# Optimization experiments

Measured on AMD Instinct MI355X. Metric: run time of the kernel, lower is better.

The kernel has to match this reference:

```python
import jax, jax.numpy as jnp
import numpy as np
from jax import lax

B, CIN, H, W = 8, 64, 128, 128
COUT, K, STRIDE, PAD = 128, 3, 1, 1
NLEV = 256  # 2**activation_bits == 2**weight_bits


def setup_inputs() -> dict:
    key = jax.random.key(0)
    kx, kw = jax.random.split(key)
    x = jax.random.uniform(kx, (B, CIN, H, W), dtype=jnp.float32)
    weight = jax.random.normal(kw, (COUT, CIN, K, K), dtype=jnp.float32)
    bias = jnp.zeros((COUT,), dtype=jnp.float32)
    return {"x": x, "weight": weight, "bias": bias}


def _lut_table(weight):
    # quantized weights in [0, 255], integer-valued
    qw = jnp.clip(jnp.round(weight * (NLEV - 1)), 0, NLEV - 1).astype(jnp.int32)
    iv = jnp.arange(NLEV, dtype=jnp.int32)
    # emulate torch .to(int16) wraparound (qw*i can exceed 32767)
    lut = (qw[..., None] * iv).astype(jnp.int16)          # [O, C, K, K, 256]
    # the original sums pcilt over its (c,p,q) dims for EVERY patch entry;
    # precollapse those dims: T[i, o] = sum_{c,p,q} lut[o,c,p,q,i]
    T = lut.astype(jnp.int32).sum(axis=(1, 2, 3))          # [O, 256]
    return T.T                                             # [256, O]


def reference(x, weight, bias):
    T = _lut_table(weight)                                 # [256, COUT]
    xq = jnp.clip(jnp.round(x * (NLEV - 1)), 0, NLEV - 1).astype(jnp.int32)
    xp = jnp.pad(xq, ((0, 0), (0, 0), (PAD, PAD), (PAD, PAD)))  # zero-pad; T[:,0]=0 matches
    xc = jnp.moveaxis(xp, 1, 0)                            # [CIN, B, Hp, Wp]

    # accumulate per-pixel channel sum of LUT rows: A[b,h,w,o] = sum_c T[x[b,c,h,w], o]
    A0 = jnp.zeros((xp.shape[0], xp.shape[2], xp.shape[3], COUT), dtype=jnp.int32)

    def body(acc, ch):
        return acc + T[ch], None

    A, _ = lax.scan(body, A0, xc)                          # [B, Hp, Wp, COUT]

    # k x k sliding-window sum over spatial dims = sum over all patch entries
    out = lax.reduce_window(A.astype(jnp.float32), 0.0, lax.add,
                            (1, K, K, 1), (1, STRIDE, STRIDE, 1), 'VALID')
    out = jnp.moveaxis(out, 3, 1) + bias[None, :, None, None]  # [B, COUT, OH, OW]
    return out
```

## Files before the change

kernel.cpp:

```cpp
#include <hip/hip_runtime.h>

#define CIN   64
#define HW    128
#define COUT  128
#define TH    8
#define TW    32
#define PXR   34
#define NITER (TH + 2)
#define NTHR  512
#define HSTR  144
#define AKSTR 136
#define SLOT  (PXR * HSTR)

#define HM_OFF    0
#define KT_OFF    19584
#define SX_OFF    35968
#define SXP_OFF   36608
#define LDS_BYTES 39872

typedef int v4i __attribute__((ext_vector_type(4)));

__device__ __forceinline__ void wg_barrier() {
  asm volatile("s_waitcnt lgkmcnt(0)\n\ts_barrier" ::: "memory");
}

__device__ __forceinline__ int quad_sum(int v) {
  v += __builtin_amdgcn_mov_dpp(v, 0xB1, 0xF, 0xF, true);
  v += __builtin_amdgcn_mov_dpp(v, 0x4E, 0xF, 0xF, true);
  return v;
}

__global__ __launch_bounds__(512)
void build_tables(const float* __restrict__ weight, int* __restrict__ W_tab,
                  char* __restrict__ Kt_g) {
  __shared__ int qw_s[576];
  __shared__ int red_s[144];
  const int o = blockIdx.x;
  const int t = threadIdx.x;
  for (int j = t; j < 576; j += 512) {
    float w = weight[o * 576 + j];
    int q = (int)rintf(w * 255.f);
    qw_s[j] = q < 0 ? 0 : (q > 255 ? 255 : q);
  }
  __syncthreads();
  const int v = t >> 2, part = t & 3;
  const int i = 128 + v;
  int cnt = 0;
  const int j0 = part * 144;
  for (int j = j0; j < j0 + 144; ++j) cnt += (qw_s[j] * i) > 32767 ? 1 : 0;
  cnt = quad_sum(cnt);
  if (part == 0) Kt_g[o * 128 + v] = (char)(cnt - 128);
  if (t < 144)
    red_s[t] = qw_s[t * 4] + qw_s[t * 4 + 1] + qw_s[t * 4 + 2] + qw_s[t * 4 + 3];
  __syncthreads();
  if (t == 0) {
    int s = 0;
    for (int kk = 0; kk < 144; ++kk) s += red_s[kk];
    W_tab[o] = s;
  }
}

__global__ __launch_bounds__(NTHR, 4)
void pcilt_main(const float* __restrict__ x, const float* __restrict__ bias,
                const int* __restrict__ W_tab, const char* __restrict__ Kt_g,
                float* __restrict__ out) {
  __shared__ uint4 ldsv[LDS_BYTES / 16];
  char* ldsb = (char*)ldsv;
  unsigned char* HmB  = (unsigned char*)(ldsb + HM_OFF);
  unsigned char* KtB  = (unsigned char*)(ldsb + KT_OFF);
  unsigned short* AK  = (unsigned short*)(ldsb + KT_OFF);
  int* Sx             = (int*)(ldsb + SX_OFF);
  int* Sxp            = (int*)(ldsb + SXP_OFF);

  const int t   = (int)threadIdx.x;
  const int bid = (int)blockIdx.x;
  const int b  = bid & 7;
  const int k  = bid >> 3;
  const int h0 = (k >> 2) * TH;
  const int w0 = (k & 3) * TW;

  for (int i = t; i < 4096; i += NTHR)
    ((unsigned int*)KtB)[i] = ((const unsigned int*)Kt_g)[i];
  {
    const uint4 z4 = make_uint4(0, 0, 0, 0);
    for (int i = t; i < 4 * SLOT / 16; i += NTHR) ((uint4*)HmB)[i] = z4;
  }

  const int l    = t & 15;
  const int slot = t >> 4;
  const int w    = t >> 6;
  const int kq   = (t >> 4) & 3;
  const int we   = t & 31;
  const int og   = t >> 5;

  float wf[8], bi[8];
#pragma unroll
  for (int m = 0; m < 8; ++m) {
    wf[m] = (float)W_tab[og * 8 + m];
    bi[m] = bias[og * 8 + m];
  }

  wg_barrier();

  v4i bfr[4][2];
  const int Mt = w >> 1, Nh = w & 1;
  if (w < 6) {
#pragma unroll
    for (int nt = 0; nt < 4; ++nt)
#pragma unroll
      for (int k64 = 0; k64 < 2; ++k64)
        bfr[nt][k64] = *(const v4i*)(KtB + (Nh * 64 + nt * 16 + l) * 128 +
                                     k64 * 64 + kq * 16);
  }

  float pf0[4], pf1[4];
  const float* xb = x + ((size_t)b * CIN + l * 4) * (HW * HW);
  const size_t cs = (size_t)HW * HW;

#define ISSUE(rn)                                                              \
  {                                                                            \
    const int iy  = h0 + (rn)-1;                                               \
    const int iyc = iy < 0 ? 0 : (iy > 127 ? 127 : iy);                        \
    const bool rok = (iy >= 0) && (iy < HW);                                   \
    int ix = w0 + slot - 1;                                                    \
    int ixc = ix < 0 ? 0 : (ix > 127 ? 127 : ix);                              \
    bool ok = rok && (ix >= 0) && (ix < HW);                                   \
    const float* xp = xb + (size_t)iyc * HW + ixc;                             \
    float v0 = xp[0], v1 = xp[cs], v2 = xp[2 * cs], v3 = xp[3 * cs];           \
    pf0[0] = ok ? v0 : 0.f; pf0[1] = ok ? v1 : 0.f;                            \
    pf0[2] = ok ? v2 : 0.f; pf0[3] = ok ? v3 : 0.f;                            \
    if (slot < 2) {                                                            \
      ix = w0 + 32 + slot - 1;                                                 \
      ixc = ix > 127 ? 127 : ix;                                               \
      ok = rok && (ix < HW);                                                   \
      const float* xq = xb + (size_t)iyc * HW + ixc;                           \
      float u0 = xq[0], u1 = xq[cs], u2 = xq[2 * cs], u3 = xq[3 * cs];         \
      pf1[0] = ok ? u0 : 0.f; pf1[1] = ok ? u1 : 0.f;                          \
      pf1[2] = ok ? u2 : 0.f; pf1[3] = ok ? u3 : 0.f;                          \
    }                                                                          \
  }

#define STAGEPX(pf, px)                                                        \
  {                                                                            \
    int q, iv0, iv1, iv2, iv3;                                                 \
    q = (int)rintf((pf)[0] * 255.f); iv0 = q < 0 ? 0 : (q > 255 ? 255 : q);    \
    q = (int)rintf((pf)[1] * 255.f); iv1 = q < 0 ? 0 : (q > 255 ? 255 : q);    \
    q = (int)rintf((pf)[2] * 255.f); iv2 = q < 0 ? 0 : (q > 255 ? 255 : q);    \
    q = (int)rintf((pf)[3] * 255.f); iv3 = q < 0 ? 0 : (q > 255 ? 255 : q);    \
    int pk = (((iv0 > 128) + (iv1 > 128) + (iv2 > 128) + (iv3 > 128)) << 20) + \
             (iv0 + iv1 + iv2 + iv3);                                          \
    pk = quad_sum(pk);                                                         \
    if ((l & 3) == 0) Sxp[sxpb + (px)*12 + (l >> 2)] = pk;                     \
    unsigned char* hp = Hc + (px)*HSTR;                                        \
    if (iv0 > 128) { int v = iv0 - 128; atomicAdd((unsigned int*)(hp + ((v >> 2) << 2)), 1u << ((v & 3) * 8)); } \
    if (iv1 > 128) { int v = iv1 - 128; atomicAdd((unsigned int*)(hp + ((v >> 2) << 2)), 1u << ((v & 3) * 8)); } \
    if (iv2 > 128) { int v = iv2 - 128; atomicAdd((unsigned int*)(hp + ((v >> 2) << 2)), 1u << ((v & 3) * 8)); } \
    if (iv3 > 128) { int v = iv3 - 128; atomicAdd((unsigned int*)(hp + ((v >> 2) << 2)), 1u << ((v & 3) * 8)); } \
  }

  ISSUE(0);

  for (int r = 0; r < NITER; ++r) {
    {
      unsigned char* Hc = HmB + (r & 3) * SLOT;
      const int sxpb = (r & 1) * (34 * 12);
      STAGEPX(pf0, slot);
      if (slot < 2) STAGEPX(pf1, 32 + slot);
      if (r + 1 < NITER) ISSUE(r + 1);
    }
    wg_barrier();

    if (r >= 2 && w < 6) {
      v4i acc[4];
#pragma unroll
      for (int nt = 0; nt < 4; ++nt) acc[nt] = (v4i){0, 0, 0, 0};
      const int prow = Mt * 16 + l;
#pragma unroll
      for (int st = 0; st < 3; ++st) {
        const unsigned char* Hs = HmB + ((r - 2 + st) & 3) * SLOT +
                                  prow * HSTR + kq * 16;
#pragma unroll
        for (int k64 = 0; k64 < 2; ++k64) {
          const v4i a = *(const v4i*)(Hs + k64 * 64);
#pragma unroll
          for (int nt = 0; nt < 4; ++nt)
            acc[nt] = __builtin_amdgcn_mfma_i32_16x16x64_i8(a, bfr[nt][k64], acc[nt], 0, 0, 0);
        }
      }
      const int pbase = Mt * 16 + kq * 4;
#pragma unroll
      for (int nt = 0; nt < 4; ++nt) {
        const int o = Nh * 64 + nt * 16 + l;
#pragma unroll
        for (int rg = 0; rg < 4; ++rg)
          AK[(pbase + rg) * AKSTR + o] = (unsigned short)acc[nt][rg];
      }
    }
    if (w == 6) {
      const int L = t - 384;
      if (L < 34) {
        const v4i sq = *(const v4i*)&Sxp[(r & 1) * (34 * 12) + L * 12];
        Sx[(r & 3) * 40 + L] = sq.x + sq.y + sq.z + sq.w;
      }
    }
    if (w == 7) {
      uint4* Hn = (uint4*)(HmB + ((r + 1) & 3) * SLOT);
      const uint4 z4 = make_uint4(0, 0, 0, 0);
      for (int i2 = t - 448; i2 < SLOT / 16; i2 += 64) Hn[i2] = z4;
    }
    wg_barrier();

    if (r >= 2) {
      const int h = h0 + r - 2;
      int v9 = 0;
#pragma unroll
      for (int q = 0; q < 3; ++q) {
        const int sl = (r - 2 + q) & 3;
        v9 += Sx[sl * 40 + we] + Sx[sl * 40 + we + 1] + Sx[sl * 40 + we + 2];
      }
      const int sx9 = v9 & 0xFFFFF;
      const int sh9 = v9 >> 20;
      int k0 = 0, k1 = 0, k2 = 0, k3 = 0, k4 = 0, k5 = 0, k6 = 0, k7 = 0;
#pragma unroll
      for (int dx = 0; dx < 3; ++dx) {
        const uint4 p = *(const uint4*)&AK[(we + dx) * AKSTR + og * 8];
        k0 += (int)(short)(p.x & 0xffffu); k1 += (int)(short)(p.x >> 16);
        k2 += (int)(short)(p.y & 0xffffu); k3 += (int)(short)(p.y >> 16);
        k4 += (int)(short)(p.z & 0xffffu); k5 += (int)(short)(p.z >> 16);
        k6 += (int)(short)(p.w & 0xffffu); k7 += (int)(short)(p.w >> 16);
      }
      const int kc = 128 * sh9;
      const float sxf = (float)sx9;
      float* op = out + (((size_t)b * COUT + og * 8) * HW + h) * HW + (w0 + we);
      const size_t os = (size_t)HW * HW;
      op[0 * os] = sxf * wf[0] - 65536.f * (float)(k0 + kc) + bi[0];
      op[1 * os] = sxf * wf[1] - 65536.f * (float)(k1 + kc) + bi[1];
      op[2 * os] = sxf * wf[2] - 65536.f * (float)(k2 + kc) + bi[2];
      op[3 * os] = sxf * wf[3] - 65536.f * (float)(k3 + kc) + bi[3];
      op[4 * os] = sxf * wf[4] - 65536.f * (float)(k4 + kc) + bi[4];
      op[5 * os] = sxf * wf[5] - 65536.f * (float)(k5 + kc) + bi[5];
      op[6 * os] = sxf * wf[6] - 65536.f * (float)(k6 + kc) + bi[6];
      op[7 * os] = sxf * wf[7] - 65536.f * (float)(k7 + kc) + bi[7];
    }
  }
}

extern "C" void kernel_launch(void* const* d_in, const int* in_sizes, int n_in,
                              void* d_out, int out_size, void* d_ws, size_t ws_size,
                              hipStream_t stream) {
  const float* x      = (const float*)d_in[0];
  const float* weight = (const float*)d_in[1];
  const float* bias   = (const float*)d_in[2];
  float* out = (float*)d_out;

  int*  W_tab = (int*)d_ws;
  char* Kt_g  = (char*)d_ws + 512;

  build_tables<<<128, 512, 0, stream>>>(weight, W_tab, Kt_g);

  pcilt_main<<<512, NTHR, 0, stream>>>(x, bias, W_tab, Kt_g, out);
}
```

Before: 43.29 us.

## Transpose AK layout with XOR swizzle and vectorize epilogue output stores

Stores the MFMA results to LDS transposed (channel-major with an XOR swizzle), packing four 16-bit values per write. The epilogue thread mapping changes so each thread owns one output channel and eight consecutive pixels, and writes them with float4 stores instead of eight scalar strided stores. The 3x3 Sx window sum moves to wave 6 and is stored once in a small LDS buffer rather than recomputed by every thread. The aim is fewer LDS transactions and better-coalesced global stores, at the cost of extra packing and swizzle arithmetic.

```diff
diff --git a/kernel.cpp b/kernel.cpp
--- a/kernel.cpp
+++ b/kernel.cpp
@@ -9,14 +9,15 @@
 #define NITER (TH + 2)
 #define NTHR  512
 #define HSTR  144
-#define AKSTR 136
 #define SLOT  (PXR * HSTR)
+#define AKS   64
 
 #define HM_OFF    0
 #define KT_OFF    19584
 #define SX_OFF    35968
 #define SXP_OFF   36608
-#define LDS_BYTES 39872
+#define SX9_OFF   39872
+#define LDS_BYTES 40064
 
 typedef int v4i __attribute__((ext_vector_type(4)));
 
@@ -71,6 +72,7 @@
   unsigned short* AK  = (unsigned short*)(ldsb + KT_OFF);
   int* Sx             = (int*)(ldsb + SX_OFF);
   int* Sxp            = (int*)(ldsb + SXP_OFF);
+  int* Sx9            = (int*)(ldsb + SX9_OFF);
 
   const int t   = (int)threadIdx.x;
   const int bid = (int)blockIdx.x;
@@ -90,15 +92,11 @@
   const int slot = t >> 4;
   const int w    = t >> 6;
   const int kq   = (t >> 4) & 3;
-  const int we   = t & 31;
-  const int og   = t >> 5;
-
-  float wf[8], bi[8];
-#pragma unroll
-  for (int m = 0; m < 8; ++m) {
-    wf[m] = (float)W_tab[og * 8 + m];
-    bi[m] = bias[og * 8 + m];
-  }
+
+  const int oe  = t & 127;
+  const int pg  = t >> 7;
+  const float wfo = (float)W_tab[oe];
+  const float bio = bias[oe];
 
   wg_barrier();
 
@@ -191,16 +189,27 @@
 #pragma unroll
       for (int nt = 0; nt < 4; ++nt) {
         const int o = Nh * 64 + nt * 16 + l;
-#pragma unroll
-        for (int rg = 0; rg < 4; ++rg)
-          AK[(pbase + rg) * AKSTR + o] = (unsigned short)acc[nt][rg];
+        const unsigned int lo = ((unsigned)acc[nt][0] & 0xFFFFu) | ((unsigned)acc[nt][1] << 16);
+        const unsigned int hi = ((unsigned)acc[nt][2] & 0xFFFFu) | ((unsigned)acc[nt][3] << 16);
+        const int sp = pbase ^ (((o >> 3) & 7) << 3);
+        *(uint2*)(AK + o * AKS + sp) = make_uint2(lo, hi);
       }
     }
     if (w == 6) {
       const int L = t - 384;
+      const int sb = (r & 1) * (34 * 12);
       if (L < 34) {
-        const v4i sq = *(const v4i*)&Sxp[(r & 1) * (34 * 12) + L * 12];
+        const v4i sq = *(const v4i*)&Sxp[sb + L * 12];
         Sx[(r & 3) * 40 + L] = sq.x + sq.y + sq.z + sq.w;
+      }
+      if (r >= 2 && L < 32) {
+        int v9 = 0;
+#pragma unroll
+        for (int q = 0; q < 3; ++q) {
+          const int sl = (r - 2 + q) & 3;
+          v9 += Sx[sl * 40 + L] + Sx[sl * 40 + L + 1] + Sx[sl * 40 + L + 2];
+        }
+        Sx9[L] = v9;
       }
     }
     if (w == 7) {
@@ -212,35 +221,29 @@
 
     if (r >= 2) {
       const int h = h0 + r - 2;
-      int v9 = 0;
-#pragma unroll
-      for (int q = 0; q < 3; ++q) {
-        const int sl = (r - 2 + q) & 3;
-        v9 += Sx[sl * 40 + we] + Sx[sl * 40 + we + 1] + Sx[sl * 40 + we + 2];
-      }
-      const int sx9 = v9 & 0xFFFFF;
-      const int sh9 = v9 >> 20;
-      int k0 = 0, k1 = 0, k2 = 0, k3 = 0, k4 = 0, k5 = 0, k6 = 0, k7 = 0;
-#pragma unroll
-      for (int dx = 0; dx < 3; ++dx) {
-        const uint4 p = *(const uint4*)&AK[(we + dx) * AKSTR + og * 8];
-        k0 += (int)(short)(p.x & 0xffffu); k1 += (int)(short)(p.x >> 16);
-        k2 += (int)(short)(p.y & 0xffffu); k3 += (int)(short)(p.y >> 16);
-        k4 += (int)(short)(p.z & 0xffffu); k5 += (int)(short)(p.z >> 16);
-        k6 += (int)(short)(p.w & 0xffffu); k7 += (int)(short)(p.w >> 16);
-      }
-      const int kc = 128 * sh9;
-      const float sxf = (float)sx9;
-      float* op = out + (((size_t)b * COUT + og * 8) * HW + h) * HW + (w0 + we);
-      const size_t os = (size_t)HW * HW;
-      op[0 * os] = sxf * wf[0] - 65536.f * (float)(k0 + kc) + bi[0];
-      op[1 * os] = sxf * wf[1] - 65536.f * (float)(k1 + kc) + bi[1];
-      op[2 * os] = sxf * wf[2] - 65536.f * (float)(k2 + kc) + bi[2];
-      op[3 * os] = sxf * wf[3] - 65536.f * (float)(k3 + kc) + bi[3];
-      op[4 * os] = sxf * wf[4] - 65536.f * (float)(k4 + kc) + bi[4];
-      op[5 * os] = sxf * wf[5] - 65536.f * (float)(k5 + kc) + bi[5];
-      op[6 * os] = sxf * wf[6] - 65536.f * (float)(k6 + kc) + bi[6];
-      op[7 * os] = sxf * wf[7] - 65536.f * (float)(k7 + kc) + bi[7];
+      const int kx = (oe >> 3) & 7;
+      const unsigned short* ar = AK + oe * AKS;
+      const uint4 A0 = *(const uint4*)(ar + ((pg ^ kx) << 3));
+      const uint4 A1 = *(const uint4*)(ar + (((pg + 1) ^ kx) << 3));
+      const v4i S0 = *(const v4i*)(Sx9 + pg * 8);
+      const v4i S1 = *(const v4i*)(Sx9 + pg * 8 + 4);
+      const unsigned int dd[5] = {A0.x, A0.y, A0.z, A0.w, A1.x};
+      int e[10];
+#pragma unroll
+      for (int i = 0; i < 10; ++i)
+        e[i] = (int)(short)((dd[i >> 1] >> ((i & 1) * 16)) & 0xFFFFu);
+      const int s[8] = {S0[0], S0[1], S0[2], S0[3], S1[0], S1[1], S1[2], S1[3]};
+      float v[8];
+#pragma unroll
+      for (int j = 0; j < 8; ++j) {
+        const int sx = s[j] & 0xFFFFF;
+        const int sh = s[j] >> 20;
+        const int k3 = e[j] + e[j + 1] + e[j + 2] + (sh << 7);
+        v[j] = (float)sx * wfo - 65536.f * (float)k3 + bio;
+      }
+      float* op = out + (((size_t)b * COUT + oe) * HW + h) * HW + w0 + pg * 8;
+      *(float4*)op       = make_float4(v[0], v[1], v[2], v[3]);
+      *(float4*)(op + 4) = make_float4(v[4], v[5], v[6], v[7]);
     }
   }
 }
```

Measured after the change: 54.47 us. 1.26x slower.

## Software-pipeline histogram, MFMA and quantization stages across rows with deeper LDS buffering

Applied to the files above, without the earlier changes.

Restructures the per-row loop into a deeper software pipeline. Quantization of the next row is separated from histogram atomics and moved after the MFMA stage, the histogram ring grows from 4 to 6 slots, and the AK output buffer is double-buffered. This removes one barrier per iteration, so histogramming row r, MFMA on older rows and quantizing row r+1 can overlap between the two barriers. The cost is more LDS (about 60KB versus 40KB), which may reduce occupancy below the launch-bounds target of 4 blocks. It also adds one extra pipeline iteration and keeps quantized values in registers.

```diff
diff --git a/kernel.cpp b/kernel.cpp
--- a/kernel.cpp
+++ b/kernel.cpp
@@ -6,17 +6,17 @@
 #define TH    8
 #define TW    32
 #define PXR   34
-#define NITER (TH + 2)
+#define NITER 11
 #define NTHR  512
 #define HSTR  144
 #define AKSTR 136
 #define SLOT  (PXR * HSTR)
 
 #define HM_OFF    0
-#define KT_OFF    19584
-#define SX_OFF    35968
-#define SXP_OFF   36608
-#define LDS_BYTES 39872
+#define AK_OFF    29376
+#define SX_OFF    55488
+#define SXP_OFF   56768
+#define LDS_BYTES 60032
 
 typedef int v4i __attribute__((ext_vector_type(4)));
 
@@ -67,8 +67,8 @@
   __shared__ uint4 ldsv[LDS_BYTES / 16];
   char* ldsb = (char*)ldsv;
   unsigned char* HmB  = (unsigned char*)(ldsb + HM_OFF);
-  unsigned char* KtB  = (unsigned char*)(ldsb + KT_OFF);
-  unsigned short* AK  = (unsigned short*)(ldsb + KT_OFF);
+  unsigned char* KtB  = (unsigned char*)(ldsb + AK_OFF);
+  unsigned short* AKB = (unsigned short*)(ldsb + AK_OFF);
   int* Sx             = (int*)(ldsb + SX_OFF);
   int* Sxp            = (int*)(ldsb + SXP_OFF);
 
@@ -83,7 +83,7 @@
     ((unsigned int*)KtB)[i] = ((const unsigned int*)Kt_g)[i];
   {
     const uint4 z4 = make_uint4(0, 0, 0, 0);
-    for (int i = t; i < 4 * SLOT / 16; i += NTHR) ((uint4*)HmB)[i] = z4;
+    for (int i = t; i < 2 * SLOT / 16; i += NTHR) ((uint4*)HmB)[i] = z4;
   }
 
   const int l    = t & 15;
@@ -114,6 +114,7 @@
   }
 
   float pf0[4], pf1[4];
+  int qv[2][8];
   const float* xb = x + ((size_t)b * CIN + l * 4) * (HW * HW);
   const size_t cs = (size_t)HW * HW;
 
@@ -129,8 +130,8 @@
     float v0 = xp[0], v1 = xp[cs], v2 = xp[2 * cs], v3 = xp[3 * cs];           \
     pf0[0] = ok ? v0 : 0.f; pf0[1] = ok ? v1 : 0.f;                            \
     pf0[2] = ok ? v2 : 0.f; pf0[3] = ok ? v3 : 0.f;                            \
-    if (slot < 2) {                                                            \
-      ix = w0 + 32 + slot - 1;                                                 \
+    if (slot >= 30) {                                                          \
+      ix = w0 + slot + 1;                                    \
       ixc = ix > 127 ? 127 : ix;                                               \
       ok = rok && (ix < HW);                                                   \
       const float* xq = xb + (size_t)iyc * HW + ixc;                           \
@@ -140,44 +141,51 @@
     }                                                                          \
   }
 
-#define STAGEPX(pf, px)                                                        \
+#define QUANT4(pf, qn, base, px, sxpb)                                         \
   {                                                                            \
-    int q, iv0, iv1, iv2, iv3;                                                 \
-    q = (int)rintf((pf)[0] * 255.f); iv0 = q < 0 ? 0 : (q > 255 ? 255 : q);    \
-    q = (int)rintf((pf)[1] * 255.f); iv1 = q < 0 ? 0 : (q > 255 ? 255 : q);    \
-    q = (int)rintf((pf)[2] * 255.f); iv2 = q < 0 ? 0 : (q > 255 ? 255 : q);    \
-    q = (int)rintf((pf)[3] * 255.f); iv3 = q < 0 ? 0 : (q > 255 ? 255 : q);    \
-    int pk = (((iv0 > 128) + (iv1 > 128) + (iv2 > 128) + (iv3 > 128)) << 20) + \
-             (iv0 + iv1 + iv2 + iv3);                                          \
+    int q;                                                                     \
+    q = (int)rintf((pf)[0] * 255.f); (qn)[(base)+0] = q < 0 ? 0 : (q > 255 ? 255 : q); \
+    q = (int)rintf((pf)[1] * 255.f); (qn)[(base)+1] = q < 0 ? 0 : (q > 255 ? 255 : q); \
+    q = (int)rintf((pf)[2] * 255.f); (qn)[(base)+2] = q < 0 ? 0 : (q > 255 ? 255 : q); \
+    q = (int)rintf((pf)[3] * 255.f); (qn)[(base)+3] = q < 0 ? 0 : (q > 255 ? 255 : q); \
+    int pk = (((qn)[(base)+0] > 128) + ((qn)[(base)+1] > 128) +                \
+              ((qn)[(base)+2] > 128) + ((qn)[(base)+3] > 128));                \
+    pk = (pk << 20) + (qn)[(base)+0] + (qn)[(base)+1] + (qn)[(base)+2] + (qn)[(base)+3]; \
     pk = quad_sum(pk);                                                         \
-    if ((l & 3) == 0) Sxp[sxpb + (px)*12 + (l >> 2)] = pk;                     \
-    unsigned char* hp = Hc + (px)*HSTR;                                        \
-    if (iv0 > 128) { int v = iv0 - 128; atomicAdd((unsigned int*)(hp + ((v >> 2) << 2)), 1u << ((v & 3) * 8)); } \
-    if (iv1 > 128) { int v = iv1 - 128; atomicAdd((unsigned int*)(hp + ((v >> 2) << 2)), 1u << ((v & 3) * 8)); } \
-    if (iv2 > 128) { int v = iv2 - 128; atomicAdd((unsigned int*)(hp + ((v >> 2) << 2)), 1u << ((v & 3) * 8)); } \
-    if (iv3 > 128) { int v = iv3 - 128; atomicAdd((unsigned int*)(hp + ((v >> 2) << 2)), 1u << ((v & 3) * 8)); } \
+    if ((l & 3) == 0) Sxp[(sxpb) + (px)*12 + (l >> 2)] = pk;                   \
+  }
+
+#define HIST4(q0, q1, q2, q3, px, Hc)                                          \
+  {                                                                            \
+    unsigned char* hp = (Hc) + (px)*HSTR;                                      \
+    if ((q0) > 128) { int v = (q0) - 128; atomicAdd((unsigned int*)(hp + ((v >> 2) << 2)), 1u << ((v & 3) * 8)); } \
+    if ((q1) > 128) { int v = (q1) - 128; atomicAdd((unsigned int*)(hp + ((v >> 2) << 2)), 1u << ((v & 3) * 8)); } \
+    if ((q2) > 128) { int v = (q2) - 128; atomicAdd((unsigned int*)(hp + ((v >> 2) << 2)), 1u << ((v & 3) * 8)); } \
+    if ((q3) > 128) { int v = (q3) - 128; atomicAdd((unsigned int*)(hp + ((v >> 2) << 2)), 1u << ((v & 3) * 8)); } \
   }
 
   ISSUE(0);
-
+  QUANT4(pf0, qv[0], 0, slot, 0);
+  if (slot >= 30) QUANT4(pf1, qv[0], 4, slot + 2, 0);
+  ISSUE(1);
+  wg_barrier();
+
+#pragma unroll
   for (int r = 0; r < NITER; ++r) {
-    {
-      unsigned char* Hc = HmB + (r & 3) * SLOT;
-      const int sxpb = (r & 1) * (34 * 12);
-      STAGEPX(pf0, slot);
-      if (slot < 2) STAGEPX(pf1, 32 + slot);
-      if (r + 1 < NITER) ISSUE(r + 1);
-    }
-    wg_barrier();
-
-    if (r >= 2 && w < 6) {
+    if (r <= 9) {
+      unsigned char* Hc = HmB + (r % 6) * SLOT;
+      const int* qc = qv[r & 1];
+      HIST4(qc[0], qc[1], qc[2], qc[3], slot, Hc);
+      if (slot >= 30) HIST4(qc[4], qc[5], qc[6], qc[7], slot + 2, Hc);
+    }
+    if (r >= 3 && w < 6) {
       v4i acc[4];
 #pragma unroll
       for (int nt = 0; nt < 4; ++nt) acc[nt] = (v4i){0, 0, 0, 0};
       const int prow = Mt * 16 + l;
 #pragma unroll
       for (int st = 0; st < 3; ++st) {
-        const unsigned char* Hs = HmB + ((r - 2 + st) & 3) * SLOT +
+        const unsigned char* Hs = HmB + ((r - 3 + st) % 6) * SLOT +
                                   prow * HSTR + kq * 16;
 #pragma unroll
         for (int k64 = 0; k64 < 2; ++k64) {
@@ -187,35 +195,45 @@
             acc[nt] = __builtin_amdgcn_mfma_i32_16x16x64_i8(a, bfr[nt][k64], acc[nt], 0, 0, 0);
         }
       }
+      unsigned short* AKw = AKB + (r & 1) * (48 * AKSTR);
       const int pbase = Mt * 16 + kq * 4;
 #pragma unroll
       for (int nt = 0; nt < 4; ++nt) {
         const int o = Nh * 64 + nt * 16 + l;
 #pragma unroll
         for (int rg = 0; rg < 4; ++rg)
-          AK[(pbase + rg) * AKSTR + o] = (unsigned short)acc[nt][rg];
-      }
-    }
-    if (w == 6) {
+          AKw[(pbase + rg) * AKSTR + o] = (unsigned short)acc[nt][rg];
+      }
+    }
+    if (w == 6 && r <= 9) {
       const int L = t - 384;
       if (L < 34) {
         const v4i sq = *(const v4i*)&Sxp[(r & 1) * (34 * 12) + L * 12];
-        Sx[(r & 3) * 40 + L] = sq.x + sq.y + sq.z + sq.w;
-      }
-    }
-    if (w == 7) {
-      uint4* Hn = (uint4*)(HmB + ((r + 1) & 3) * SLOT);
+        Sx[(r & 7) * 40 + L] = sq.x + sq.y + sq.z + sq.w;
+      }
+    }
+    if (w == 7 && r <= 7) {
+      uint4* Hn = (uint4*)(HmB + ((r + 2) % 6) * SLOT);
       const uint4 z4 = make_uint4(0, 0, 0, 0);
       for (int i2 = t - 448; i2 < SLOT / 16; i2 += 64) Hn[i2] = z4;
     }
+    if (r <= 8) {
+      const int sxpb = ((r + 1) & 1) * (34 * 12);
+      int* qn = qv[(r + 1) & 1];
+      QUANT4(pf0, qn, 0, slot, sxpb);
+      if (slot >= 30) QUANT4(pf1, qn, 4, slot + 2, sxpb);
+    }
+    if (r <= 7) ISSUE(r + 2);
+
     wg_barrier();
 
-    if (r >= 2) {
-      const int h = h0 + r - 2;
+    if (r >= 3) {
+      const int h = h0 + r - 3;
+      const unsigned short* AKr = AKB + (r & 1) * (48 * AKSTR);
       int v9 = 0;
 #pragma unroll
       for (int q = 0; q < 3; ++q) {
-        const int sl = (r - 2 + q) & 3;
+        const int sl = (r - 3 + q) & 7;
         v9 += Sx[sl * 40 + we] + Sx[sl * 40 + we + 1] + Sx[sl * 40 + we + 2];
       }
       const int sx9 = v9 & 0xFFFFF;
@@ -223,7 +241,7 @@
       int k0 = 0, k1 = 0, k2 = 0, k3 = 0, k4 = 0, k5 = 0, k6 = 0, k7 = 0;
 #pragma unroll
       for (int dx = 0; dx < 3; ++dx) {
-        const uint4 p = *(const uint4*)&AK[(we + dx) * AKSTR + og * 8];
+        const uint4 p = *(const uint4*)&AKr[(we + dx) * AKSTR + og * 8];
         k0 += (int)(short)(p.x & 0xffffu); k1 += (int)(short)(p.x >> 16);
         k2 += (int)(short)(p.y & 0xffffu); k3 += (int)(short)(p.y >> 16);
         k4 += (int)(short)(p.z & 0xffffu); k5 += (int)(short)(p.z >> 16);
```

Result: slower. 44.45 us (+2.7%).
